# Kernel tuning notes

Measured on AMD Instinct MI355X. Metric: run time of the kernel, lower is better.

Reference implementation:

```python
import jax, jax.numpy as jnp
import numpy as np

FACTOR = 5


def setup_inputs() -> dict:
    key = jax.random.key(0)
    k1, k2, k3, k4 = jax.random.split(key, 4)
    B, L, H, D = 2, 4096, 8, 64
    sample_k = min(FACTOR * int(np.ceil(np.log(L))), L)  # 45
    return {
        "queries": jax.random.normal(k1, (B, L, H, D), dtype=jnp.float32),
        "keys": jax.random.normal(k2, (B, L, H, D), dtype=jnp.float32),
        "values": jax.random.normal(k3, (B, L, H, D), dtype=jnp.float32),
        "attn_mask": jnp.zeros((1,), dtype=bool),  # unused; ProbMask is built internally
        "index_sample": jax.random.randint(k4, (L, sample_k), 0, L, dtype=jnp.int32),
    }


def reference(queries, keys, values, attn_mask, index_sample):
    # queries/keys/values: [B, L, H, D] -> [B, H, L, D]
    Q = jnp.swapaxes(queries, 1, 2)
    K = jnp.swapaxes(keys, 1, 2)
    V = jnp.swapaxes(values, 1, 2)
    B, H, L_Q, D = Q.shape
    L_K = K.shape[2]
    n_top = min(FACTOR * int(np.ceil(np.log(L_Q))), L_Q)
    scale = 1.0 / jnp.sqrt(jnp.float32(D))

    # --- sparse measurement: sampled QK scores ---
    # K_sample[b,h,q,s,d] = K[b,h,index_sample[q,s],d]
    K_sample = K[:, :, index_sample, :]                       # [B,H,L_Q,S,D]
    QK_sample = jnp.einsum("bhqd,bhqsd->bhqs", Q, K_sample)   # [B,H,L_Q,S]
    M = QK_sample.max(axis=-1) - QK_sample.sum(axis=-1) / L_K  # sparsity measure

    # --- top-u query selection ---
    _, M_top = jax.lax.top_k(M, n_top)                         # [B,H,u]
    Q_reduce = jnp.take_along_axis(Q, M_top[..., None], axis=2)  # [B,H,u,D]

    # --- full scores for selected queries ---
    scores = jnp.einsum("bhud,bhkd->bhuk", Q_reduce, K) * scale  # [B,H,u,L_K]

    # mask_flag=True: causal ProbMask (key pos > selected query pos)
    key_pos = jnp.arange(L_K)
    causal = key_pos[None, None, None, :] > M_top[..., None]
    scores = jnp.where(causal, -jnp.inf, scores)
    attn = jax.nn.softmax(scores, axis=-1)

    # --- initial context (cumsum, masked case) + scatter update ---
    context = jnp.cumsum(V, axis=2)                            # [B,H,L_Q,D]
    ctx_sel = jnp.einsum("bhuk,bhkd->bhud", attn, V)
    b_idx = jnp.arange(B)[:, None, None]
    h_idx = jnp.arange(H)[None, :, None]
    context = context.at[b_idx, h_idx, M_top].set(ctx_sel)
    return jnp.swapaxes(context, 1, 2)  # [B, L_Q, H, D]
```

## Files before the change

kernel.cpp:

```cpp
#include <hip/hip_runtime.h>
#include <math.h>

#define B_    2
#define L_    4096
#define H_    8
#define D_    64
#define S_    45
#define NT_   45
#define BH_   16
#define CHV   64
#define NCHV  64
#define KC    128
#define SCALE 0.125f
#define NEG_BIG (-1e30f)

#define OFF_M     0
#define OFF_MTOP  65536
#define OFF_T     66304
#define OFF_CTX   67072
#define OFF_VSUM  131072
#define NZERO     46848

typedef __attribute__((ext_vector_type(8))) short s8b;
typedef __attribute__((ext_vector_type(4))) float f32x4;

template <int CTRL>
__device__ __forceinline__ float dpp_ror_f(float x) {
    int y = __builtin_amdgcn_update_dpp(0, __float_as_int(x), CTRL, 0xF, 0xF, false);
    return __int_as_float(y);
}
template <int CTRL>
__device__ __forceinline__ int dpp_ror_i(int x) {
    return __builtin_amdgcn_update_dpp(0, x, CTRL, 0xF, 0xF, false);
}

__device__ __forceinline__ unsigned f2bf(float x) {
    return (__float_as_uint(x) >> 16);
}
__device__ __forceinline__ float bflo(unsigned u) { return __uint_as_float(u << 16); }
__device__ __forceinline__ float bfhi(unsigned u) { return __uint_as_float(u & 0xffff0000u); }

__global__ __launch_bounds__(256) void k1(const float* __restrict__ Q,
                                          const float* __restrict__ Kt,
                                          const float* __restrict__ V,
                                          const int* __restrict__ samp,
                                          float* __restrict__ ws)
{
    int tid  = threadIdx.x;
    int w    = tid >> 6;
    int lane = tid & 63;

    if (blockIdx.x < 4096) {
        int i   = blockIdx.x;
        int xcd = i & 7;
        int b   = xcd >> 2;
        int hh  = (xcd >> 1) & 1;
        int qq  = ((i >> 3) << 1) | (xcd & 1);

        __shared__ int soff[4][S_];
        if (tid < 4 * S_) {
            int qs = tid / S_, ss = tid - qs * S_;
            soff[qs][ss] = (samp[(qq * 4 + qs) * S_ + ss] << 11) | (hh << 10);
        }
        __syncthreads();

        int q  = qq * 4 + w;
        int h4 = lane >> 4;

        const float4 q4 = *(const float4*)(Q +
            ((((long)b * L_ + q) * H_ + hh * 4) << 6) + lane * 4);

        const char* kslab = (const char*)Kt + (long)b * (L_ * 2048);
        unsigned lb = (unsigned)(lane * 16);

        float mx = NEG_BIG, sm = 0.f;
#pragma unroll
        for (int jb = 0; jb < 45; jb += 15) {
            float4 kb[15];
#pragma unroll
            for (int j = 0; j < 15; ++j)
                kb[j] = *(const float4*)(kslab +
                        ((unsigned)soff[w][jb + j] + lb));
#pragma unroll
            for (int j = 0; j < 15; ++j) {
                float p = q4.x * kb[j].x + q4.y * kb[j].y +
                          q4.z * kb[j].z + q4.w * kb[j].w;
                p += dpp_ror_f<0x121>(p);
                p += dpp_ror_f<0x122>(p);
                p += dpp_ror_f<0x124>(p);
                p += dpp_ror_f<0x128>(p);
                mx = fmaxf(mx, p);
                sm += p;
            }
        }
        if ((lane & 15) == 0)
            ws[OFF_M + ((long)(b * 8 + hh * 4 + h4)) * L_ + q] =
                mx - sm * (1.0f / (float)L_);
    } else {
        int unit = (blockIdx.x - 4096) * 4 + w;
        int bh = unit >> 6, ch = unit & 63;
        int b = bh >> 3, h = bh & 7;
        const float* vp = V + ((((long)b * L_ + (long)ch * CHV) * H_ + h) << 6) + lane;
        float ssum = 0.f;
#pragma unroll
        for (int ib = 0; ib < CHV; ib += 16) {
            float vb[16];
#pragma unroll
            for (int j = 0; j < 16; ++j) vb[j] = vp[(long)(ib + j) * (H_ * D_)];
#pragma unroll
            for (int j = 0; j < 16; ++j) ssum += vb[j];
        }
        ws[OFF_VSUM + unit * 64 + lane] = ssum;
    }
}

__global__ __launch_bounds__(256) void k2(float* __restrict__ ws)
{
    int tid  = threadIdx.x;
    int lane = tid & 63;

    for (int i = blockIdx.x * 256 + tid; i < NZERO; i += 16 * 256)
        ws[OFF_T + i] = 0.f;
    if (tid >= 64) return;

    int bh = blockIdx.x;

    const uint4* m4 = (const uint4*)(ws + OFF_M + (long)bh * L_ + lane * 64);
    unsigned key[64];
#pragma unroll
    for (int j4 = 0; j4 < 16; ++j4) {
        uint4 kv = m4[j4];
        unsigned uu[4] = {kv.x, kv.y, kv.z, kv.w};
#pragma unroll
        for (int e = 0; e < 4; ++e) {
            unsigned u = uu[e];
            key[j4 * 4 + e] = (u & 0x80000000u) ? ~u : (u | 0x80000000u);
        }
    }

    unsigned lo = 0u, hi = 0xFFFFFFFFu;
    for (int it = 0; it < 32; ++it) {
        unsigned d = hi - lo;
        unsigned mid = lo + (d >> 1) + (d & 1);
        int cnt = 0;
#pragma unroll
        for (int j = 0; j < 64; ++j) cnt += (key[j] >= mid) ? 1 : 0;
        cnt += dpp_ror_i<0x121>(cnt);
        cnt += dpp_ror_i<0x122>(cnt);
        cnt += dpp_ror_i<0x124>(cnt);
        cnt += dpp_ror_i<0x128>(cnt);
        cnt += __shfl_xor(cnt, 16);
        cnt += __shfl_xor(cnt, 32);
        if (cnt >= NT_) lo = mid; else hi = mid - 1;
    }
    unsigned lam = lo;

    int cgt = 0, ceq = 0;
#pragma unroll
    for (int j = 0; j < 64; ++j) {
        cgt += (key[j] > lam) ? 1 : 0;
        ceq += (key[j] == lam) ? 1 : 0;
    }
    int packed = (cgt << 16) | ceq;
    int incl = packed;
#pragma unroll
    for (int off = 1; off < 64; off <<= 1) {
        int t = __shfl_up(incl, off);
        if (lane >= off) incl += t;
    }
    int excl = incl - packed;
    int ngt_total = __shfl(incl, 63) >> 16;

    int* Mtop = (int*)ws + OFF_MTOP + bh * NT_;
    int gpos = excl >> 16;
    int epos = ngt_total + (excl & 0xFFFF);
#pragma unroll
    for (int j = 0; j < 64; ++j) {
        if (key[j] > lam) {
            Mtop[gpos++] = lane * 64 + j;
        } else if (key[j] == lam) {
            if (epos < NT_) Mtop[epos] = lane * 64 + j;
            ++epos;
        }
    }
}

#define KPAD16 72
#define PSTR   136
__global__ __launch_bounds__(256) void k3(const float* __restrict__ Q,
                                          const float* __restrict__ Kt,
                                          const float* __restrict__ V,
                                          float* __restrict__ out,
                                          float* __restrict__ ws)
{
    __shared__ unsigned short Klds16[KC * KPAD16];
    __shared__ unsigned short Qs16[32 * KPAD16];
    __shared__ unsigned short P16[32 * PSTR];
    __shared__ int qposs[32];

    int tid = threadIdx.x;

    if (blockIdx.x < 1024) {
        int bh = blockIdx.x >> 6;
        int kc = (blockIdx.x >> 1) & 31;
        int ug = blockIdx.x & 1;
        int b = bh >> 3, h = bh & 7;
        int kbase = kc * KC;
        int u0 = ug * 23;
        int NU = ug ? 22 : 23;

        if (tid < 32) {
            int uu = tid < NU ? tid : NU - 1;
            qposs[tid] = ((const int*)ws)[OFF_MTOP + bh * NT_ + u0 + uu];
        }
        __syncthreads();

        {
            const float4* ksrc4 = (const float4*)(Kt + ((((long)b * L_ + kbase) * H_ + h) << 6));
#pragma unroll
            for (int i = 0; i < 8; ++i) {
                int e = i * 256 + tid;
                int r = e >> 4, c4 = e & 15;
                float4 kv = ksrc4[(long)r * (H_ * D_ / 4) + c4];
                uint2 pk;
                pk.x = (__float_as_uint(kv.x) >> 16) | (__float_as_uint(kv.y) & 0xffff0000u);
                pk.y = (__float_as_uint(kv.z) >> 16) | (__float_as_uint(kv.w) & 0xffff0000u);
                *(uint2*)&Klds16[r * KPAD16 + ((c4 * 4) ^ ((r & 7) << 3))] = pk;
            }
#pragma unroll
            for (int i = 0; i < 2; ++i) {
                int e = i * 256 + tid;
                int r = e >> 4, c4 = e & 15;
                int qp = qposs[r];
                const float4* qsrc4 = (const float4*)(Q + ((((long)b * L_ + qp) * H_ + h) << 6));
                float4 qv = qsrc4[c4];
                uint2 pk;
                pk.x = (__float_as_uint(qv.x) >> 16) | (__float_as_uint(qv.y) & 0xffff0000u);
                pk.y = (__float_as_uint(qv.z) >> 16) | (__float_as_uint(qv.w) & 0xffff0000u);
                *(uint2*)&Qs16[r * KPAD16 + ((c4 * 4) ^ ((r & 7) << 3))] = pk;
            }
        }
        __syncthreads();

        {
            int lane = tid & 63, w = tid >> 6;
            int c = lane & 15, hi = lane >> 4;
            int t = w & 1, Hh = w >> 1;
            int slot = t * 16 + c;
            int qp = qposs[slot];

            s8b bq0 = *(const s8b*)&Qs16[slot * KPAD16 + ((hi * 8) ^ ((slot & 7) << 3))];
            s8b bq1 = *(const s8b*)&Qs16[slot * KPAD16 + ((32 + hi * 8) ^ ((slot & 7) << 3))];

            f32x4 acc0 = {0.f,0.f,0.f,0.f}, acc1 = acc0, acc2 = acc0, acc3 = acc0;
#define QK_TILE(MT, ACC)                                                      \
            {                                                                 \
                int kr = Hh * 64 + (MT) * 16 + c;                             \
                s8b a0 = *(const s8b*)&Klds16[kr * KPAD16 +                   \
                            ((hi * 8) ^ ((kr & 7) << 3))];                    \
                s8b a1 = *(const s8b*)&Klds16[kr * KPAD16 +                   \
                            ((32 + hi * 8) ^ ((kr & 7) << 3))];               \
                ACC = __builtin_amdgcn_mfma_f32_16x16x32_bf16(a0, bq0, ACC, 0, 0, 0); \
                ACC = __builtin_amdgcn_mfma_f32_16x16x32_bf16(a1, bq1, ACC, 0, 0, 0); \
            }
            QK_TILE(0, acc0)
            QK_TILE(1, acc1)
            QK_TILE(2, acc2)
            QK_TILE(3, acc3)
#undef QK_TILE

            float ssum = 0.f;
#pragma unroll
            for (int mt = 0; mt < 4; ++mt) {
                f32x4 a = mt == 0 ? acc0 : (mt == 1 ? acc1 : (mt == 2 ? acc2 : acc3));
                float e[4];
#pragma unroll
                for (int reg = 0; reg < 4; ++reg) {
                    int kpos = kbase + Hh * 64 + mt * 16 + hi * 4 + reg;
                    e[reg] = (kpos > qp) ? 0.f : __expf(a[reg] * SCALE);
                    ssum += e[reg];
                }
                uint2 pk;
                pk.x = f2bf(e[0]) | (f2bf(e[1]) << 16);
                pk.y = f2bf(e[2]) | (f2bf(e[3]) << 16);
                *(uint2*)&P16[slot * PSTR + Hh * 64 + mt * 16 + hi * 4] = pk;
            }
            ssum += __shfl_xor(ssum, 16);
            ssum += __shfl_xor(ssum, 32);
            if (hi == 0) {
                int sl = t * 16 + c;
                if (sl < NU)
                    atomicAdd(&ws[OFF_T + bh * NT_ + u0 + sl], ssum);
            }
        }
        __syncthreads();

        {
            int lane = tid & 63, w = tid >> 6;
            int c = lane & 15, hi = lane >> 4;
            const float* vsrc = V + ((((long)b * L_ + kbase) * H_ + h) << 6)
                                  + (w * 16 + c);
            f32x4 pacc0 = {0.f,0.f,0.f,0.f}, pacc1 = pacc0;
#pragma unroll
            for (int ks = 0; ks < 4; ++ks) {
                float vf[8];
#pragma unroll
                for (int j = 0; j < 8; ++j)
                    vf[j] = vsrc[(long)(ks * 32 + hi * 8 + j) * (H_ * D_)];
                uint4 uv;
                uv.x = (__float_as_uint(vf[0]) >> 16) | (__float_as_uint(vf[1]) & 0xffff0000u);
                uv.y = (__float_as_uint(vf[2]) >> 16) | (__float_as_uint(vf[3]) & 0xffff0000u);
                uv.z = (__float_as_uint(vf[4]) >> 16) | (__float_as_uint(vf[5]) & 0xffff0000u);
                uv.w = (__float_as_uint(vf[6]) >> 16) | (__float_as_uint(vf[7]) & 0xffff0000u);
                s8b bv = *(s8b*)&uv;
                s8b a0 = *(const s8b*)&P16[(c)      * PSTR + ks * 32 + hi * 8];
                s8b a1 = *(const s8b*)&P16[(16 + c) * PSTR + ks * 32 + hi * 8];
                pacc0 = __builtin_amdgcn_mfma_f32_16x16x32_bf16(a0, bv, pacc0, 0, 0, 0);
                pacc1 = __builtin_amdgcn_mfma_f32_16x16x32_bf16(a1, bv, pacc1, 0, 0, 0);
            }
#pragma unroll
            for (int reg = 0; reg < 4; ++reg) {
                int ua = hi * 4 + reg;
                if (ua < NU)
                    atomicAdd(&ws[OFF_CTX + ((long)(bh * NT_ + u0 + ua) << 6)
                                  + w * 16 + c], pacc0[reg]);
                int ub = 16 + hi * 4 + reg;
                if (ub < NU)
                    atomicAdd(&ws[OFF_CTX + ((long)(bh * NT_ + u0 + ub) << 6)
                                  + w * 16 + c], pacc1[reg]);
            }
        }
    } else {
        int w    = tid >> 6;
        int lane = tid & 63;
        int unit = (blockIdx.x - 1024) * 4 + w;
        int bh = unit >> 6, ch = unit & 63;
        int b = bh >> 3, h = bh & 7;
        int d = lane;

        float acc = 0.f;
        {
            const float* vs = ws + OFF_VSUM + (long)bh * NCHV * 64 + d;
            int c = 0;
            for (; c + 8 <= ch; c += 8) {
                float vb[8];
#pragma unroll
                for (int j = 0; j < 8; ++j) vb[j] = vs[(c + j) * 64];
#pragma unroll
                for (int j = 0; j < 8; ++j) acc += vb[j];
            }
            for (; c < ch; ++c) acc += vs[c * 64];
        }

        const float* vp = V   + ((((long)b * L_ + (long)ch * CHV) * H_ + h) << 6) + d;
        float*       op = out + ((((long)b * L_ + (long)ch * CHV) * H_ + h) << 6) + d;
#pragma unroll
        for (int ib = 0; ib < CHV; ib += 16) {
            float vb[16];
#pragma unroll
            for (int j = 0; j < 16; ++j) vb[j] = vp[(long)(ib + j) * (H_ * D_)];
#pragma unroll
            for (int j = 0; j < 16; ++j) {
                acc += vb[j];
                op[(long)(ib + j) * (H_ * D_)] = acc;
            }
        }
    }
}

__global__ __launch_bounds__(256) void kD(float* __restrict__ out,
                                          const float* __restrict__ ws)
{
    int tid  = threadIdx.x;
    int w    = tid >> 6;
    int lane = tid & 63;
    int unit = blockIdx.x * 4 + w;
    int bh = unit / NT_;
    int b = bh >> 3, h = bh & 7;

    float T   = ws[OFF_T + unit];
    float ctx = ws[OFF_CTX + ((long)unit << 6) + lane];
    int   qp  = ((const int*)ws)[OFF_MTOP + unit];
    out[((((long)b * L_ + qp) * H_ + h) << 6) + lane] = ctx / T;
}

extern "C" void kernel_launch(void* const* d_in, const int* in_sizes, int n_in,
                              void* d_out, int out_size, void* d_ws, size_t ws_size,
                              hipStream_t stream)
{
    const float* Q    = (const float*)d_in[0];
    const float* K    = (const float*)d_in[1];
    const float* V    = (const float*)d_in[2];
    const int*   samp = (const int*)d_in[4];
    float* out = (float*)d_out;
    float* ws  = (float*)d_ws;

    k1<<<4352, 256, 0, stream>>>(Q, K, V, samp, ws);
    k2<<<16, 256, 0, stream>>>(ws);
    k3<<<1280, 256, 0, stream>>>(Q, K, V, out, ws);
    kD<<<180, 256, 0, stream>>>(out, ws);
}
```

Measured before the change: 166.9 us.

## Prefetch V into registers early and load Q fragments directly from global

All 32 V elements per thread are loaded into registers at kernel start, so their global latency overlaps the K staging and QK phase instead of sitting on the critical path of the PV MFMA loop. The Q operand fragments are now read straight from global into registers, which removes the Qs16 and qposs shared buffers and one __syncthreads. The cost is extra register pressure from 32 live floats and the Q fragments, which may reduce occupancy.

```diff
diff --git a/kernel.cpp b/kernel.cpp
--- a/kernel.cpp
+++ b/kernel.cpp
@@ -194,9 +194,7 @@
                                           float* __restrict__ ws)
 {
     __shared__ unsigned short Klds16[KC * KPAD16];
-    __shared__ unsigned short Qs16[32 * KPAD16];
     __shared__ unsigned short P16[32 * PSTR];
-    __shared__ int qposs[32];
 
     int tid = threadIdx.x;
 
@@ -209,11 +207,40 @@
         int u0 = ug * 23;
         int NU = ug ? 22 : 23;
 
-        if (tid < 32) {
-            int uu = tid < NU ? tid : NU - 1;
-            qposs[tid] = ((const int*)ws)[OFF_MTOP + bh * NT_ + u0 + uu];
-        }
-        __syncthreads();
+        int lane = tid & 63, w = tid >> 6;
+        int c = lane & 15, hi = lane >> 4;
+        int t = w & 1, Hh = w >> 1;
+        int slot = t * 16 + c;
+
+        int qp = ((const int*)ws)[OFF_MTOP + bh * NT_ + u0 +
+                                  (slot < NU ? slot : NU - 1)];
+
+        const float* vsrc = V + ((((long)b * L_ + kbase) * H_ + h) << 6)
+                              + (w * 16 + c);
+        float vf[32];
+#pragma unroll
+        for (int ks = 0; ks < 4; ++ks)
+#pragma unroll
+            for (int j = 0; j < 8; ++j)
+                vf[ks * 8 + j] = vsrc[(long)(ks * 32 + hi * 8 + j) * (H_ * D_)];
+
+        s8b bq0, bq1;
+        {
+            const float4* qrow = (const float4*)(Q + ((((long)b * L_ + qp) * H_ + h) << 6));
+            float4 qa = qrow[hi * 2], qb = qrow[hi * 2 + 1];
+            float4 qc = qrow[8 + hi * 2], qd = qrow[8 + hi * 2 + 1];
+            uint4 u0v, u1v;
+            u0v.x = (__float_as_uint(qa.x) >> 16) | (__float_as_uint(qa.y) & 0xffff0000u);
+            u0v.y = (__float_as_uint(qa.z) >> 16) | (__float_as_uint(qa.w) & 0xffff0000u);
+            u0v.z = (__float_as_uint(qb.x) >> 16) | (__float_as_uint(qb.y) & 0xffff0000u);
+            u0v.w = (__float_as_uint(qb.z) >> 16) | (__float_as_uint(qb.w) & 0xffff0000u);
+            u1v.x = (__float_as_uint(qc.x) >> 16) | (__float_as_uint(qc.y) & 0xffff0000u);
+            u1v.y = (__float_as_uint(qc.z) >> 16) | (__float_as_uint(qc.w) & 0xffff0000u);
+            u1v.z = (__float_as_uint(qd.x) >> 16) | (__float_as_uint(qd.y) & 0xffff0000u);
+            u1v.w = (__float_as_uint(qd.z) >> 16) | (__float_as_uint(qd.w) & 0xffff0000u);
+            bq0 = *(s8b*)&u0v;
+            bq1 = *(s8b*)&u1v;
+        }
 
         {
             const float4* ksrc4 = (const float4*)(Kt + ((((long)b * L_ + kbase) * H_ + h) << 6));
@@ -227,31 +254,10 @@
                 pk.y = (__float_as_uint(kv.z) >> 16) | (__float_as_uint(kv.w) & 0xffff0000u);
                 *(uint2*)&Klds16[r * KPAD16 + ((c4 * 4) ^ ((r & 7) << 3))] = pk;
             }
-#pragma unroll
-            for (int i = 0; i < 2; ++i) {
-                int e = i * 256 + tid;
-                int r = e >> 4, c4 = e & 15;
-                int qp = qposs[r];
-                const float4* qsrc4 = (const float4*)(Q + ((((long)b * L_ + qp) * H_ + h) << 6));
-                float4 qv = qsrc4[c4];
-                uint2 pk;
-                pk.x = (__float_as_uint(qv.x) >> 16) | (__float_as_uint(qv.y) & 0xffff0000u);
-                pk.y = (__float_as_uint(qv.z) >> 16) | (__float_as_uint(qv.w) & 0xffff0000u);
-                *(uint2*)&Qs16[r * KPAD16 + ((c4 * 4) ^ ((r & 7) << 3))] = pk;
-            }
         }
         __syncthreads();
 
         {
-            int lane = tid & 63, w = tid >> 6;
-            int c = lane & 15, hi = lane >> 4;
-            int t = w & 1, Hh = w >> 1;
-            int slot = t * 16 + c;
-            int qp = qposs[slot];
-
-            s8b bq0 = *(const s8b*)&Qs16[slot * KPAD16 + ((hi * 8) ^ ((slot & 7) << 3))];
-            s8b bq1 = *(const s8b*)&Qs16[slot * KPAD16 + ((32 + hi * 8) ^ ((slot & 7) << 3))];
-
             f32x4 acc0 = {0.f,0.f,0.f,0.f}, acc1 = acc0, acc2 = acc0, acc3 = acc0;
 #define QK_TILE(MT, ACC)                                                      \
             {                                                                 \
@@ -287,31 +293,20 @@
             }
             ssum += __shfl_xor(ssum, 16);
             ssum += __shfl_xor(ssum, 32);
-            if (hi == 0) {
-                int sl = t * 16 + c;
-                if (sl < NU)
-                    atomicAdd(&ws[OFF_T + bh * NT_ + u0 + sl], ssum);
-            }
+            if (hi == 0 && slot < NU)
+                atomicAdd(&ws[OFF_T + bh * NT_ + u0 + slot], ssum);
         }
         __syncthreads();
 
         {
-            int lane = tid & 63, w = tid >> 6;
-            int c = lane & 15, hi = lane >> 4;
-            const float* vsrc = V + ((((long)b * L_ + kbase) * H_ + h) << 6)
-                                  + (w * 16 + c);
             f32x4 pacc0 = {0.f,0.f,0.f,0.f}, pacc1 = pacc0;
 #pragma unroll
             for (int ks = 0; ks < 4; ++ks) {
-                float vf[8];
-#pragma unroll
-                for (int j = 0; j < 8; ++j)
-                    vf[j] = vsrc[(long)(ks * 32 + hi * 8 + j) * (H_ * D_)];
                 uint4 uv;
-                uv.x = (__float_as_uint(vf[0]) >> 16) | (__float_as_uint(vf[1]) & 0xffff0000u);
-                uv.y = (__float_as_uint(vf[2]) >> 16) | (__float_as_uint(vf[3]) & 0xffff0000u);
-                uv.z = (__float_as_uint(vf[4]) >> 16) | (__float_as_uint(vf[5]) & 0xffff0000u);
-                uv.w = (__float_as_uint(vf[6]) >> 16) | (__float_as_uint(vf[7]) & 0xffff0000u);
+                uv.x = (__float_as_uint(vf[ks*8+0]) >> 16) | (__float_as_uint(vf[ks*8+1]) & 0xffff0000u);
+                uv.y = (__float_as_uint(vf[ks*8+2]) >> 16) | (__float_as_uint(vf[ks*8+3]) & 0xffff0000u);
+                uv.z = (__float_as_uint(vf[ks*8+4]) >> 16) | (__float_as_uint(vf[ks*8+5]) & 0xffff0000u);
+                uv.w = (__float_as_uint(vf[ks*8+6]) >> 16) | (__float_as_uint(vf[ks*8+7]) & 0xffff0000u);
                 s8b bv = *(s8b*)&uv;
                 s8b a0 = *(const s8b*)&P16[(c)      * PSTR + ks * 32 + hi * 8];
                 s8b a1 = *(const s8b*)&P16[(16 + c) * PSTR + ks * 32 + hi * 8];
```

Result: no change. 167.7 us (+0.5%).
